# Kernel optimization log

Measured on AMD Instinct MI355X. Metric: run time of the kernel, lower is better.

Reference implementation:

```python
import jax, jax.numpy as jnp
import numpy as np
import math

D_MODEL = 1024
NUM_HEADS = 16


def setup_inputs() -> dict:
    key = jax.random.key(0)
    ks = jax.random.split(key, 5)
    B, S, D = 4, 2048, D_MODEL
    scale = 1.0 / math.sqrt(D)
    x = jax.random.normal(ks[0], (B, S, D), dtype=jnp.float32)
    wq = jax.random.normal(ks[1], (D, D), dtype=jnp.float32) * scale
    wk = jax.random.normal(ks[2], (D, D), dtype=jnp.float32) * scale
    wv = jax.random.normal(ks[3], (D, D), dtype=jnp.float32) * scale
    wo = jax.random.normal(ks[4], (D, D), dtype=jnp.float32) * scale
    return {"x": x, "wq": wq, "wk": wk, "wv": wv, "wo": wo}


def _mhsa(x, wq, wk, wv, wo):
    B, S, D = x.shape
    H = NUM_HEADS
    dk = D // H
    # projections: y = x @ W^T
    q = (x @ wq.T).reshape(B, S, H, dk).transpose(0, 2, 1, 3)  # [B,H,S,dk]
    k = (x @ wk.T).reshape(B, S, H, dk).transpose(0, 2, 1, 3)
    v = (x @ wv.T).reshape(B, S, H, dk).transpose(0, 2, 1, 3)
    scores = jnp.einsum("bhqd,bhkd->bhqk", q, k) / jnp.sqrt(jnp.asarray(dk, x.dtype))
    mask = jnp.tril(jnp.ones((S, S), dtype=bool))  # [S,S] causal
    neg_inf = jnp.asarray(-jnp.inf, scores.dtype)
    scores_masked = jnp.where(mask, scores, neg_inf)
    max_scores = jnp.max(scores_masked, axis=-1, keepdims=True)
    max_scores = jnp.where(jnp.isfinite(max_scores), max_scores, jnp.zeros_like(max_scores))
    exp_scores = jnp.exp(scores - max_scores) * mask.astype(scores.dtype)
    denom = jnp.maximum(exp_scores.sum(axis=-1, keepdims=True), 1e-9)
    attn = exp_scores / denom
    out = jnp.einsum("bhqk,bhkd->bhqd", attn, v)  # [B,H,S,dk]
    out = out.transpose(0, 2, 1, 3).reshape(B, S, D)
    return out @ wo.T


def reference(x, wq, wk, wv, wo):
    return _mhsa(x, wq, wk, wv, wo)
```

## Files before the change

kernel.cpp:

```cpp
#include <hip/hip_runtime.h>
#include <stdint.h>


typedef __attribute__((ext_vector_type(8))) short short8;
typedef __attribute__((ext_vector_type(4))) short short4v;
typedef __attribute__((ext_vector_type(4))) float float4v;
typedef __attribute__((ext_vector_type(2))) unsigned int uint2v;

#define QSCALE 0.18033688011112042f
#define EXP_C2 5.770780163555852f

__device__ inline short f2bf(float f) {
  union { float f; uint32_t u; } v; v.f = f;
  uint32_t r = (v.u + 0x7fffu + ((v.u >> 16) & 1)) >> 16;
  return (short)(uint16_t)r;
}

__device__ inline unsigned int pack2bf(float a, float b) {
  union { float f; unsigned int u; } ua, ub;
  ua.f = a; ub.f = b;
  return __builtin_amdgcn_perm(ub.u, ua.u, 0x07060302u);
}

__device__ inline void async_copy16(const void* g, void* l) {
  __builtin_amdgcn_global_load_lds(
      (const __attribute__((address_space(1))) void*)g,
      (__attribute__((address_space(3))) void*)l, 16, 0, 0);
}

__global__ __launch_bounds__(256) void cvtAll(
    const float* __restrict__ x, const float* __restrict__ wq,
    const float* __restrict__ wk, const float* __restrict__ wv,
    const float* __restrict__ wo,
    short* __restrict__ xb, short* __restrict__ wqb, short* __restrict__ wkb,
    short* __restrict__ wvb, short* __restrict__ wob) {
  const int b = blockIdx.x;
  const float* s; short* d; int base;
  if (b < 8192) { s = x; d = xb; base = b; }
  else {
    const int wi = (b - 8192) >> 10; base = (b - 8192) & 1023;
    s = (wi == 0) ? wq : (wi == 1) ? wk : (wi == 2) ? wv : wo;
    d = (wi == 0) ? wqb : (wi == 1) ? wkb : (wi == 2) ? wvb : wob;
  }
  const size_t i = (size_t)base * 256 + threadIdx.x;
  const float4v v = *(const float4v*)(s + 4 * i);
  short4v o;
  o[0] = f2bf(v[0]); o[1] = f2bf(v[1]);
  o[2] = f2bf(v[2]); o[3] = f2bf(v[3]);
  *(short4v*)(d + 4 * i) = o;
}

template <int MODE>
__global__ __launch_bounds__(256) void gemm_bt(
    const short* __restrict__ A,
    const short* __restrict__ W0, const short* __restrict__ W1,
    const short* __restrict__ W2,
    short* __restrict__ Yb0, short* __restrict__ Yb1, short* __restrict__ Yb2,
    float* __restrict__ Yf) {
  constexpr int Kd = 1024;
  __shared__ __align__(16) short As[2][128 * 32];
  __shared__ __align__(16) short Bs[2][128 * 32];

  const int t = threadIdx.x;
  const int w = t >> 6, l = t & 63, l15 = l & 15, quad = l >> 4;
  const int wm = w >> 1, wn = w & 1;

  int mblk, nblk, zz = 0;
  {
    const int o = blockIdx.x;
    const int xcd = o & 7, slot = o >> 3;
    mblk = (xcd << 3) | (slot & 7);
    const int c = slot >> 3;
    if (MODE == 0) { nblk = c & 7; zz = c >> 3; }
    else nblk = c;
  }
  const int m0 = mblk * 128, n0 = nblk * 128;

  const short* W = W0;
  short* Yb = Yb0;
  float sc = 1.0f;
  if (MODE == 0) {
    if (zz == 0) sc = QSCALE;
    else if (zz == 1) { W = W1; Yb = Yb1; }
    else { W = W2; Yb = Yb2; }
  }

  float4v acc[4][4];
#pragma unroll
  for (int i = 0; i < 4; i++)
#pragma unroll
    for (int j = 0; j < 4; j++) acc[i][j] = (float4v){0.f, 0.f, 0.f, 0.f};

  const int r4 = t >> 2, c48 = (t & 3) * 8;
  const short* Wbase = W + (n0 + r4) * Kd + c48;
  const int ldsW = w * 512;
  const int i0 = m0 + r4;
  const int i1 = m0 + 64 + r4;

  auto STAGE = [&](int k0, int b) {
    if (MODE == 0) {
      async_copy16(A + (size_t)i0 * Kd + k0 + c48, &As[b][ldsW]);
      async_copy16(A + (size_t)i1 * Kd + k0 + c48, &As[b][ldsW + 2048]);
    } else {
      const int k = k0 + c48, h = k >> 6, dd = k & 63;
      async_copy16(A + ((((size_t)(i0 >> 11) * 16 + h) * 2048 + (i0 & 2047)) * 64 + dd),
                   &As[b][ldsW]);
      async_copy16(A + ((((size_t)(i1 >> 11) * 16 + h) * 2048 + (i1 & 2047)) * 64 + dd),
                   &As[b][ldsW + 2048]);
    }
    async_copy16(Wbase + k0, &Bs[b][ldsW]);
    async_copy16(Wbase + 64 * Kd + k0, &Bs[b][ldsW + 2048]);
  };

  STAGE(0, 0);
  __syncthreads();

  for (int k0 = 0; k0 < Kd; k0 += 32) {
    const int cur = (k0 >> 5) & 1;
    if (k0 + 32 < Kd) STAGE(k0 + 32, cur ^ 1);
    short8 af[4], bf[4];
#pragma unroll
    for (int mi = 0; mi < 4; mi++)
      af[mi] = *(const short8*)&As[cur][(wm * 64 + mi * 16 + l15) * 32 + quad * 8];
#pragma unroll
    for (int ni = 0; ni < 4; ni++)
      bf[ni] = *(const short8*)&Bs[cur][(wn * 64 + ni * 16 + l15) * 32 + quad * 8];
#pragma unroll
    for (int mi = 0; mi < 4; mi++)
#pragma unroll
      for (int ni = 0; ni < 4; ni++)
        acc[mi][ni] = __builtin_amdgcn_mfma_f32_16x16x32_bf16(
            af[mi], bf[ni], acc[mi][ni], 0, 0, 0);
    __syncthreads();
  }

#pragma unroll
  for (int mi = 0; mi < 4; mi++) {
    const int ib = m0 + wm * 64 + mi * 16 + quad * 4;
#pragma unroll
    for (int ni = 0; ni < 4; ni++) {
      const int j = n0 + wn * 64 + ni * 16 + l15;
#pragma unroll
      for (int r = 0; r < 4; r++) {
        const int i = ib + r;
        if (MODE == 0) {
          Yb[((((size_t)(i >> 11) * 16 + (j >> 6)) * 2048 + (i & 2047)) * 64 + (j & 63))] =
              f2bf(acc[mi][ni][r] * sc);
        } else {
          Yf[(size_t)i * 1024 + j] = acc[mi][ni][r];
        }
      }
    }
  }
}

__global__ __launch_bounds__(256) void transV(const short* __restrict__ V,
                                              short* __restrict__ VT) {
  __shared__ __align__(16) short Ls[64 * 72];
  const int t = threadIdx.x;
  const int s0 = blockIdx.x * 64, bh = blockIdx.y;
  const short* Vh = V + (size_t)bh * 2048 * 64;
  short* Th = VT + (size_t)bh * 64 * 2048;
  const int r = t >> 2, c = (t & 3) * 16;
  *(short8*)&Ls[r * 72 + c] = *(const short8*)&Vh[(size_t)(s0 + r) * 64 + c];
  *(short8*)&Ls[r * 72 + c + 8] = *(const short8*)&Vh[(size_t)(s0 + r) * 64 + c + 8];
  __syncthreads();
  short8 o0, o1;
#pragma unroll
  for (int j = 0; j < 8; j++) {
    o0[j] = Ls[(c + j) * 72 + r];
    o1[j] = Ls[(c + 8 + j) * 72 + r];
  }
  *(short8*)&Th[(size_t)r * 2048 + s0 + c] = o0;
  *(short8*)&Th[(size_t)r * 2048 + s0 + c + 8] = o1;
}

__global__ __launch_bounds__(256) void attn4(
    short* __restrict__ Q,
    const short* __restrict__ K,
    const short* __restrict__ VT) {
  __shared__ __align__(16) short Ks[2][64 * 64];
  __shared__ __align__(16) short Vs[2][64 * 64];
  __shared__ __align__(16) short Ps[4][16 * 64];

  const int t = threadIdx.x;
  const int w = t >> 6, l = t & 63, l15 = l & 15, quad = l >> 4;
  const int bh = blockIdx.x;
  const int qp = blockIdx.y;
  short* Qh = Q + (size_t)bh * 2048 * 64;
  const short* Kh = K + (size_t)bh * 2048 * 64;
  const short* Vh = VT + (size_t)bh * 64 * 2048;

  const int sr = t >> 2, c0 = t & 3;
  const int ssw = sr & 7;
  const int stA = sr * 64 + (((2 * c0) ^ ssw) << 3);
  const int stB = sr * 64 + (((2 * c0 + 1) ^ ssw) << 3);
  const int gA = c0 * 16, gB = c0 * 16 + 8;

  const int fsw = l15 & 7;
  const int fc0 = (quad ^ fsw) << 3;
  const int fc1 = ((4 + quad) ^ fsw) << 3;
  short* PsW = &Ps[w][0];
  const int pwr = l15 * 64;

  short8 ones;
#pragma unroll
  for (int j = 0; j < 8; j++) ones[j] = (short)0x3F80;
  const float4v initC = (float4v){-EXP_C2, -EXP_C2, -EXP_C2, -EXP_C2};

  for (int pass = 0; pass < 2; pass++) {
    const int q0 = (pass ? (31 - qp) : qp) * 64;
    const int qn = q0 + w * 16 + l15;
    const short8 qf0 = *(const short8*)&Qh[(size_t)qn * 64 + quad * 8];
    const short8 qf1 = *(const short8*)&Qh[(size_t)qn * 64 + 32 + quad * 8];

    float4v acc[4];
#pragma unroll
    for (int dt = 0; dt < 4; dt++) acc[dt] = (float4v){0.f, 0.f, 0.f, 0.f};
    float4v accL = (float4v){0.f, 0.f, 0.f, 0.f};

    short8 kv0 = *(const short8*)&Kh[(size_t)sr * 64 + gA];
    short8 kv1 = *(const short8*)&Kh[(size_t)sr * 64 + gB];
    short8 vv0 = *(const short8*)&Vh[(size_t)sr * 2048 + gA];
    short8 vv1 = *(const short8*)&Vh[(size_t)sr * 2048 + gB];

    int p = 0;
    for (int kb = 0; kb <= q0; kb += 64, p ^= 1) {
      const bool diag = (kb == q0);
      short* KsP = &Ks[p][0];
      short* VsP = &Vs[p][0];
      *(short8*)&KsP[stA] = kv0;
      *(short8*)&KsP[stB] = kv1;
      *(short8*)&VsP[stA] = vv0;
      *(short8*)&VsP[stB] = vv1;
      __syncthreads();

      const int kb2 = diag ? kb : kb + 64;
      kv0 = *(const short8*)&Kh[(size_t)(kb2 + sr) * 64 + gA];
      kv1 = *(const short8*)&Kh[(size_t)(kb2 + sr) * 64 + gB];
      vv0 = *(const short8*)&Vh[(size_t)sr * 2048 + kb2 + gA];
      vv1 = *(const short8*)&Vh[(size_t)sr * 2048 + kb2 + gB];

#pragma unroll
      for (int kt = 0; kt < 4; kt++) {
        const int krb = (kt * 16 + l15) * 64;
        const short8 kf0 = *(const short8*)&KsP[krb + fc0];
        const short8 kf1 = *(const short8*)&KsP[krb + fc1];
        __builtin_amdgcn_s_setprio(1);
        float4v s = __builtin_amdgcn_mfma_f32_16x16x32_bf16(kf0, qf0, initC, 0, 0, 0);
        s = __builtin_amdgcn_mfma_f32_16x16x32_bf16(kf1, qf1, s, 0, 0, 0);
        __builtin_amdgcn_s_setprio(0);
        float p0 = __builtin_amdgcn_exp2f(s[0]);
        float p1 = __builtin_amdgcn_exp2f(s[1]);
        float p2 = __builtin_amdgcn_exp2f(s[2]);
        float p3 = __builtin_amdgcn_exp2f(s[3]);
        if (diag) {
          const int key = kb + kt * 16 + quad * 4;
          p0 = (key <= qn) ? p0 : 0.f;
          p1 = (key + 1 <= qn) ? p1 : 0.f;
          p2 = (key + 2 <= qn) ? p2 : 0.f;
          p3 = (key + 3 <= qn) ? p3 : 0.f;
        }
        uint2v pw;
        pw[0] = pack2bf(p0, p1);
        pw[1] = pack2bf(p2, p3);
        *(uint2v*)&PsW[pwr + (((2 * kt + (quad >> 1)) ^ fsw) << 3) +
                       ((quad & 1) << 2)] = pw;
      }
      __builtin_amdgcn_wave_barrier();

      const short8 pf0 = *(const short8*)&PsW[pwr + fc0];
      const short8 pf1 = *(const short8*)&PsW[pwr + fc1];
      __builtin_amdgcn_s_setprio(1);
#pragma unroll
      for (int dt = 0; dt < 4; dt++) {
        const int vrb = (dt * 16 + l15) * 64;
        const short8 vf0 = *(const short8*)&VsP[vrb + fc0];
        const short8 vf1 = *(const short8*)&VsP[vrb + fc1];
        acc[dt] = __builtin_amdgcn_mfma_f32_16x16x32_bf16(vf0, pf0, acc[dt], 0, 0, 0);
        acc[dt] = __builtin_amdgcn_mfma_f32_16x16x32_bf16(vf1, pf1, acc[dt], 0, 0, 0);
      }
      accL = __builtin_amdgcn_mfma_f32_16x16x32_bf16(ones, pf0, accL, 0, 0, 0);
      accL = __builtin_amdgcn_mfma_f32_16x16x32_bf16(ones, pf1, accL, 0, 0, 0);
      __builtin_amdgcn_s_setprio(0);
    }

    const float inv = 1.0f / fmaxf(accL[0], 1e-30f);
#pragma unroll
    for (int dt = 0; dt < 4; dt++) {
      short4v o;
#pragma unroll
      for (int ri = 0; ri < 4; ri++) o[ri] = f2bf(acc[dt][ri] * inv);
      *(short4v*)&Qh[(size_t)qn * 64 + dt * 16 + quad * 4] = o;
    }
    if (pass == 0) __syncthreads();
  }
}

extern "C" void kernel_launch(void* const* d_in, const int* in_sizes, int n_in,
                              void* d_out, int out_size, void* d_ws,
                              size_t ws_size, hipStream_t stream) {
  const float* x = (const float*)d_in[0];
  const float* wq = (const float*)d_in[1];
  const float* wk = (const float*)d_in[2];
  const float* wv = (const float*)d_in[3];
  const float* wo = (const float*)d_in[4];
  float* out = (float*)d_out;

  short* xb = (short*)d_out;
  short* vtg = xb + (size_t)8192 * 1024;

  short* wqb = (short*)d_ws;
  short* wkb = wqb + (size_t)1024 * 1024;
  short* wvb = wkb + (size_t)1024 * 1024;
  short* wob = wvb + (size_t)1024 * 1024;
  short* qws = wob + (size_t)1024 * 1024;
  short* kws = qws + (size_t)8192 * 1024;
  short* vws = kws + (size_t)8192 * 1024;

  cvtAll<<<12288, 256, 0, stream>>>(x, wq, wk, wv, wo, xb, wqb, wkb, wvb, wob);
  gemm_bt<0><<<1536, 256, 0, stream>>>(
      xb, wqb, wkb, wvb, qws, kws, vws, nullptr);
  transV<<<dim3(32, 64), 256, 0, stream>>>(vws, vtg);
  attn4<<<dim3(64, 16), 256, 0, stream>>>(qws, kws, vtg);
  gemm_bt<1><<<512, 256, 0, stream>>>(
      qws, wob, nullptr, nullptr, nullptr, nullptr, nullptr, out);
}
```

Before: 243.0 us.

## Fuse fp32-to-bf16 conversion of x into the QKV projection GEMM

The separate conversion pass over x (8192x1024 fp32) is removed. The QKV GEMM now loads fp32 x directly into registers, converts it with packed bf16 instructions, and writes it to LDS as part of the double-buffered pipeline. This saves one full read and write of x plus the bf16 re-read, but x is now read three times in fp32 (once per Q/K/V z-slice) and A-tile staging goes through registers instead of async LDS copies.

```diff
diff --git a/kernel.cpp b/kernel.cpp
--- a/kernel.cpp
+++ b/kernel.cpp
@@ -6,6 +6,7 @@
 typedef __attribute__((ext_vector_type(4))) short short4v;
 typedef __attribute__((ext_vector_type(4))) float float4v;
 typedef __attribute__((ext_vector_type(2))) unsigned int uint2v;
+typedef __attribute__((ext_vector_type(4))) unsigned int uint4v;
 
 #define QSCALE 0.18033688011112042f
 #define EXP_C2 5.770780163555852f
@@ -22,26 +23,27 @@
   return __builtin_amdgcn_perm(ub.u, ua.u, 0x07060302u);
 }
 
+__device__ inline unsigned int cvtpk(float a, float b) {
+  unsigned int r;
+  asm("v_cvt_pk_bf16_f32 %0, %1, %2" : "=v"(r) : "v"(a), "v"(b));
+  return r;
+}
+
 __device__ inline void async_copy16(const void* g, void* l) {
   __builtin_amdgcn_global_load_lds(
       (const __attribute__((address_space(1))) void*)g,
       (__attribute__((address_space(3))) void*)l, 16, 0, 0);
 }
 
-__global__ __launch_bounds__(256) void cvtAll(
-    const float* __restrict__ x, const float* __restrict__ wq,
-    const float* __restrict__ wk, const float* __restrict__ wv,
-    const float* __restrict__ wo,
-    short* __restrict__ xb, short* __restrict__ wqb, short* __restrict__ wkb,
+__global__ __launch_bounds__(256) void cvtW(
+    const float* __restrict__ wq, const float* __restrict__ wk,
+    const float* __restrict__ wv, const float* __restrict__ wo,
+    short* __restrict__ wqb, short* __restrict__ wkb,
     short* __restrict__ wvb, short* __restrict__ wob) {
   const int b = blockIdx.x;
-  const float* s; short* d; int base;
-  if (b < 8192) { s = x; d = xb; base = b; }
-  else {
-    const int wi = (b - 8192) >> 10; base = (b - 8192) & 1023;
-    s = (wi == 0) ? wq : (wi == 1) ? wk : (wi == 2) ? wv : wo;
-    d = (wi == 0) ? wqb : (wi == 1) ? wkb : (wi == 2) ? wvb : wob;
-  }
+  const int wi = b >> 10, base = b & 1023;
+  const float* s = (wi == 0) ? wq : (wi == 1) ? wk : (wi == 2) ? wv : wo;
+  short* d = (wi == 0) ? wqb : (wi == 1) ? wkb : (wi == 2) ? wvb : wob;
   const size_t i = (size_t)base * 256 + threadIdx.x;
   const float4v v = *(const float4v*)(s + 4 * i);
   short4v o;
@@ -52,6 +54,7 @@
 
 template <int MODE>
 __global__ __launch_bounds__(256) void gemm_bt(
+    const float* __restrict__ Xf,
     const short* __restrict__ A,
     const short* __restrict__ W0, const short* __restrict__ W1,
     const short* __restrict__ W2,
@@ -96,12 +99,13 @@
   const int ldsW = w * 512;
   const int i0 = m0 + r4;
   const int i1 = m0 + 64 + r4;
-
-  auto STAGE = [&](int k0, int b) {
-    if (MODE == 0) {
-      async_copy16(A + (size_t)i0 * Kd + k0 + c48, &As[b][ldsW]);
-      async_copy16(A + (size_t)i1 * Kd + k0 + c48, &As[b][ldsW + 2048]);
-    } else {
+  const float* X0 = Xf + (size_t)i0 * Kd + c48;
+  const float* X1 = Xf + (size_t)i1 * Kd + c48;
+
+  float4v a0, a1, a2, a3;
+
+  auto STAGE_ASYNC = [&](int k0, int b) {
+    if (MODE == 1) {
       const int k = k0 + c48, h = k >> 6, dd = k & 63;
       async_copy16(A + ((((size_t)(i0 >> 11) * 16 + h) * 2048 + (i0 & 2047)) * 64 + dd),
                    &As[b][ldsW]);
@@ -111,13 +115,33 @@
     async_copy16(Wbase + k0, &Bs[b][ldsW]);
     async_copy16(Wbase + 64 * Kd + k0, &Bs[b][ldsW + 2048]);
   };
-
-  STAGE(0, 0);
+  auto LOADA = [&](int k0) {
+    a0 = *(const float4v*)(X0 + k0);
+    a1 = *(const float4v*)(X0 + k0 + 4);
+    a2 = *(const float4v*)(X1 + k0);
+    a3 = *(const float4v*)(X1 + k0 + 4);
+  };
+  auto WRITEA = [&](int b) {
+    uint4v u0, u1;
+    u0[0] = cvtpk(a0[0], a0[1]); u0[1] = cvtpk(a0[2], a0[3]);
+    u0[2] = cvtpk(a1[0], a1[1]); u0[3] = cvtpk(a1[2], a1[3]);
+    u1[0] = cvtpk(a2[0], a2[1]); u1[1] = cvtpk(a2[2], a2[3]);
+    u1[2] = cvtpk(a3[0], a3[1]); u1[3] = cvtpk(a3[2], a3[3]);
+    *(uint4v*)&As[b][8 * t] = u0;
+    *(uint4v*)&As[b][2048 + 8 * t] = u1;
+  };
+
+  STAGE_ASYNC(0, 0);
+  if (MODE == 0) { LOADA(0); WRITEA(0); }
   __syncthreads();
 
   for (int k0 = 0; k0 < Kd; k0 += 32) {
-    const int cur = (k0 >> 5) & 1;
-    if (k0 + 32 < Kd) STAGE(k0 + 32, cur ^ 1);
+    const int cur = (k0 >> 5) & 1, nxt = cur ^ 1;
+    const bool pre = (k0 + 32 < Kd);
+    if (pre) {
+      STAGE_ASYNC(k0 + 32, nxt);
+      if (MODE == 0) LOADA(k0 + 32);
+    }
     short8 af[4], bf[4];
 #pragma unroll
     for (int mi = 0; mi < 4; mi++)
@@ -131,6 +155,7 @@
       for (int ni = 0; ni < 4; ni++)
         acc[mi][ni] = __builtin_amdgcn_mfma_f32_16x16x32_bf16(
             af[mi], bf[ni], acc[mi][ni], 0, 0, 0);
+    if (MODE == 0 && pre) WRITEA(nxt);
     __syncthreads();
   }
 
@@ -307,8 +332,7 @@
   const float* wo = (const float*)d_in[4];
   float* out = (float*)d_out;
 
-  short* xb = (short*)d_out;
-  short* vtg = xb + (size_t)8192 * 1024;
+  short* vtg = (short*)d_out;
 
   short* wqb = (short*)d_ws;
   short* wkb = wqb + (size_t)1024 * 1024;
@@ -318,11 +342,11 @@
   short* kws = qws + (size_t)8192 * 1024;
   short* vws = kws + (size_t)8192 * 1024;
 
-  cvtAll<<<12288, 256, 0, stream>>>(x, wq, wk, wv, wo, xb, wqb, wkb, wvb, wob);
+  cvtW<<<4096, 256, 0, stream>>>(wq, wk, wv, wo, wqb, wkb, wvb, wob);
   gemm_bt<0><<<1536, 256, 0, stream>>>(
-      xb, wqb, wkb, wvb, qws, kws, vws, nullptr);
+      x, nullptr, wqb, wkb, wvb, qws, kws, vws, nullptr);
   transV<<<dim3(32, 64), 256, 0, stream>>>(vws, vtg);
   attn4<<<dim3(64, 16), 256, 0, stream>>>(qws, kws, vtg);
   gemm_bt<1><<<512, 256, 0, stream>>>(
-      qws, wob, nullptr, nullptr, nullptr, nullptr, nullptr, out);
-}
+      nullptr, qws, wob, nullptr, nullptr, nullptr, nullptr, nullptr, out);
+}
```

Measured after the change: 254.5 us. 4.8% more time.

## Triple-buffer GEMM LDS tiles with swizzled layout and single barrier per step

Applied to the files above, without the earlier changes.

Switches the projection GEMM's shared-memory staging from double to triple buffering. Each k-step now waits with a partial vmcnt instead of a full __syncthreads, so one tile load can stay in flight while the current tile is consumed. The LDS tile is repacked into a 64-wide XOR-swizzled layout to cut bank conflicts on the fragment reads. This uses more LDS, which could lower occupancy, and depends on the vmcnt count being right for correctness.

```diff
diff --git a/kernel.cpp b/kernel.cpp
--- a/kernel.cpp
+++ b/kernel.cpp
@@ -58,8 +58,8 @@
     short* __restrict__ Yb0, short* __restrict__ Yb1, short* __restrict__ Yb2,
     float* __restrict__ Yf) {
   constexpr int Kd = 1024;
-  __shared__ __align__(16) short As[2][128 * 32];
-  __shared__ __align__(16) short Bs[2][128 * 32];
+  __shared__ __align__(16) short As[3][64 * 64];
+  __shared__ __align__(16) short Bs[3][64 * 64];
 
   const int t = threadIdx.x;
   const int w = t >> 6, l = t & 63, l15 = l & 15, quad = l >> 4;
@@ -91,47 +91,65 @@
 #pragma unroll
     for (int j = 0; j < 4; j++) acc[i][j] = (float4v){0.f, 0.f, 0.f, 0.f};
 
-  const int r4 = t >> 2, c48 = (t & 3) * 8;
-  const short* Wbase = W + (n0 + r4) * Kd + c48;
+  const int rr = t >> 3;
+  const int u = (t & 7) ^ (rr & 7);
+  const int mo = rr + ((u >> 2) << 6);
+  const int ko = (u & 3) * 8;
   const int ldsW = w * 512;
-  const int i0 = m0 + r4;
-  const int i1 = m0 + 64 + r4;
+
+  const short* Wp1 = W + (size_t)(n0 + mo) * Kd + ko;
+  const short* Wp2 = W + (size_t)(n0 + 32 + mo) * Kd + ko;
+  const short* Ap1 = A + (size_t)(m0 + mo) * Kd + ko;
+  const short* Ap2 = A + (size_t)(m0 + 32 + mo) * Kd + ko;
+  const int iA1 = m0 + mo, iA2 = m0 + 32 + mo;
 
   auto STAGE = [&](int k0, int b) {
     if (MODE == 0) {
-      async_copy16(A + (size_t)i0 * Kd + k0 + c48, &As[b][ldsW]);
-      async_copy16(A + (size_t)i1 * Kd + k0 + c48, &As[b][ldsW + 2048]);
+      async_copy16(Ap1 + k0, &As[b][ldsW]);
+      async_copy16(Ap2 + k0, &As[b][2048 + ldsW]);
     } else {
-      const int k = k0 + c48, h = k >> 6, dd = k & 63;
-      async_copy16(A + ((((size_t)(i0 >> 11) * 16 + h) * 2048 + (i0 & 2047)) * 64 + dd),
+      const int k = k0 + ko, h = k >> 6, dd = k & 63;
+      async_copy16(A + ((((size_t)(iA1 >> 11) * 16 + h) * 2048 + (iA1 & 2047)) * 64 + dd),
                    &As[b][ldsW]);
-      async_copy16(A + ((((size_t)(i1 >> 11) * 16 + h) * 2048 + (i1 & 2047)) * 64 + dd),
-                   &As[b][ldsW + 2048]);
-    }
-    async_copy16(Wbase + k0, &Bs[b][ldsW]);
-    async_copy16(Wbase + 64 * Kd + k0, &Bs[b][ldsW + 2048]);
+      async_copy16(A + ((((size_t)(iA2 >> 11) * 16 + h) * 2048 + (iA2 & 2047)) * 64 + dd),
+                   &As[b][2048 + ldsW]);
+    }
+    async_copy16(Wp1 + k0, &Bs[b][ldsW]);
+    async_copy16(Wp2 + k0, &Bs[b][2048 + ldsW]);
   };
 
+  const int swz = l15 & 7;
+  const int aCh = (((wm << 2) | quad) ^ swz) << 3;
+  const int bCh = (((wn << 2) | quad) ^ swz) << 3;
+  const int rB = l15 * 64;
+
   STAGE(0, 0);
-  __syncthreads();
-
+
+  int cur = 0;
   for (int k0 = 0; k0 < Kd; k0 += 32) {
-    const int cur = (k0 >> 5) & 1;
-    if (k0 + 32 < Kd) STAGE(k0 + 32, cur ^ 1);
+    const int nxt = (cur == 2) ? 0 : cur + 1;
+    if (k0 + 32 < Kd) {
+      STAGE(k0 + 32, nxt);
+      asm volatile("s_waitcnt vmcnt(4)" ::: "memory");
+    } else {
+      asm volatile("s_waitcnt vmcnt(0)" ::: "memory");
+    }
+    __builtin_amdgcn_s_barrier();
+
     short8 af[4], bf[4];
 #pragma unroll
     for (int mi = 0; mi < 4; mi++)
-      af[mi] = *(const short8*)&As[cur][(wm * 64 + mi * 16 + l15) * 32 + quad * 8];
+      af[mi] = *(const short8*)&As[cur][mi * 1024 + rB + aCh];
 #pragma unroll
     for (int ni = 0; ni < 4; ni++)
-      bf[ni] = *(const short8*)&Bs[cur][(wn * 64 + ni * 16 + l15) * 32 + quad * 8];
+      bf[ni] = *(const short8*)&Bs[cur][ni * 1024 + rB + bCh];
 #pragma unroll
     for (int mi = 0; mi < 4; mi++)
 #pragma unroll
       for (int ni = 0; ni < 4; ni++)
         acc[mi][ni] = __builtin_amdgcn_mfma_f32_16x16x32_bf16(
             af[mi], bf[ni], acc[mi][ni], 0, 0, 0);
-    __syncthreads();
+    cur = nxt;
   }
 
 #pragma unroll
```

New measurement: 249.3 us. 2.6% more time.

## Add 8-wave 256x128 QKV projection GEMM with swizzled LDS and split-phase pipelining

Applied to the files above, without the earlier changes.

Replaces the QKV projection GEMM with a dedicated kernel using 512 threads, 256x128 tiles, and a 64-wide K step split into two 32-wide sub-phases. It adds an XOR-swizzled LDS layout, explicit vmcnt waits with raw barriers so loads overlap MFMA work, and s_setprio around the MFMA blocks. The goal is better operand reuse, fewer LDS bank conflicts and fewer full syncs in the largest GEMM. The cost is more LDS per block and hand-tuned waitcnt logic that must match the number of copies in flight.

```diff
diff --git a/kernel.cpp b/kernel.cpp
--- a/kernel.cpp
+++ b/kernel.cpp
@@ -50,12 +50,126 @@
   *(short4v*)(d + 4 * i) = o;
 }
 
+__global__ __launch_bounds__(512) void gemm_qkv8(
+    const short* __restrict__ A,
+    const short* __restrict__ W0, const short* __restrict__ W1,
+    const short* __restrict__ W2,
+    short* __restrict__ Yb0, short* __restrict__ Yb1, short* __restrict__ Yb2) {
+  constexpr int Kd = 1024;
+  __shared__ __align__(16) short As[2 * 2 * 2 * 4096];
+  __shared__ __align__(16) short Bs[2 * 2 * 4096];
+
+  const int t = threadIdx.x;
+  const int wv = t >> 6, l = t & 63, l15 = l & 15, quad = l >> 4;
+  const int wm = wv >> 1, wn = wv & 1;
+
+  int mblk, nblk, zz;
+  {
+    const int o = blockIdx.x;
+    const int xcd = o & 7, slot = o >> 3;
+    mblk = (xcd << 2) | (slot & 3);
+    const int c = slot >> 2;
+    nblk = c & 7; zz = c >> 3;
+  }
+  const int m0 = mblk * 256, n0 = nblk * 128;
+
+  const short* W = W0;
+  short* Yb = Yb0;
+  float sc = 1.0f;
+  if (zz == 0) sc = QSCALE;
+  else if (zz == 1) { W = W1; Yb = Yb1; }
+  else { W = W2; Yb = Yb2; }
+
+  float4v acc[4][4];
+#pragma unroll
+  for (int i = 0; i < 4; i++)
+#pragma unroll
+    for (int j = 0; j < 4; j++) acc[i][j] = (float4v){0.f, 0.f, 0.f, 0.f};
+
+  const int rr = t >> 3, j8 = t & 7;
+  const int u = j8 ^ (rr & 7);
+  const int mo = rr + ((u >> 2) << 6);
+  const int ko = (u & 3) * 8;
+  const int dstW = wv * 512;
+
+  const short* Asrc0 = A + (size_t)(m0 + mo) * Kd + ko;
+  const short* Asrc1 = A + (size_t)(m0 + 128 + mo) * Kd + ko;
+  const short* Bsrc = W + (size_t)(n0 + mo) * Kd + ko;
+
+  auto STAGE_S = [&](int kbase, int b, int s) {
+    async_copy16(Asrc0 + kbase, &As[((b * 2 + s) * 2 + 0) * 4096 + dstW]);
+    async_copy16(Asrc1 + kbase, &As[((b * 2 + s) * 2 + 1) * 4096 + dstW]);
+    async_copy16(Bsrc + kbase, &Bs[(b * 2 + s) * 4096 + dstW]);
+  };
+
+  const int swz = l15 & 7;
+  const int aBase = (wm >> 1) * 4096 + l15 * 64 +
+                    (((((wm & 1) << 2) | quad) ^ swz) << 3);
+  const int bBase = l15 * 64 + ((((wn << 2) | quad) ^ swz) << 3);
+
+  auto PHASE = [&](int cur, int sl) {
+    const int ab = cur * 16384 + sl * 8192 + aBase;
+    const int bb = cur * 8192 + sl * 4096 + bBase;
+    short8 af[4], bf[4];
+#pragma unroll
+    for (int mi = 0; mi < 4; mi++) af[mi] = *(const short8*)&As[ab + mi * 1024];
+#pragma unroll
+    for (int ni = 0; ni < 4; ni++) bf[ni] = *(const short8*)&Bs[bb + ni * 1024];
+    __builtin_amdgcn_s_setprio(1);
+#pragma unroll
+    for (int mi = 0; mi < 4; mi++)
+#pragma unroll
+      for (int ni = 0; ni < 4; ni++)
+        acc[mi][ni] = __builtin_amdgcn_mfma_f32_16x16x32_bf16(
+            af[mi], bf[ni], acc[mi][ni], 0, 0, 0);
+    __builtin_amdgcn_s_setprio(0);
+  };
+
+  STAGE_S(0, 0, 0);
+  STAGE_S(32, 0, 1);
+
+  for (int kt = 0; kt < 16; ++kt) {
+    const int cur = kt & 1, nb = cur ^ 1;
+    const int k0 = kt * 64;
+    const bool last = (kt == 15);
+
+    if (!last) {
+      STAGE_S(k0 + 64, nb, 0);
+      asm volatile("s_waitcnt vmcnt(3)" ::: "memory");
+    } else {
+      asm volatile("s_waitcnt vmcnt(0)" ::: "memory");
+    }
+    __builtin_amdgcn_s_barrier();
+    __builtin_amdgcn_sched_barrier(0);
+    PHASE(cur, 0);
+
+    if (!last) STAGE_S(k0 + 96, nb, 1);
+    PHASE(cur, 1);
+
+    __builtin_amdgcn_s_barrier();
+    __builtin_amdgcn_sched_barrier(0);
+  }
+
+#pragma unroll
+  for (int mi = 0; mi < 4; mi++) {
+    const int ib = m0 + wm * 64 + mi * 16 + quad * 4;
+#pragma unroll
+    for (int ni = 0; ni < 4; ni++) {
+      const int j = n0 + wn * 64 + ni * 16 + l15;
+#pragma unroll
+      for (int r = 0; r < 4; r++) {
+        const int i = ib + r;
+        Yb[((((size_t)(i >> 11) * 16 + (j >> 6)) * 2048 + (i & 2047)) * 64 + (j & 63))] =
+            f2bf(acc[mi][ni][r] * sc);
+      }
+    }
+  }
+}
+
 template <int MODE>
 __global__ __launch_bounds__(256) void gemm_bt(
     const short* __restrict__ A,
-    const short* __restrict__ W0, const short* __restrict__ W1,
-    const short* __restrict__ W2,
-    short* __restrict__ Yb0, short* __restrict__ Yb1, short* __restrict__ Yb2,
+    const short* __restrict__ W0,
     float* __restrict__ Yf) {
   constexpr int Kd = 1024;
   __shared__ __align__(16) short As[2][128 * 32];
@@ -65,25 +179,16 @@
   const int w = t >> 6, l = t & 63, l15 = l & 15, quad = l >> 4;
   const int wm = w >> 1, wn = w & 1;
 
-  int mblk, nblk, zz = 0;
+  int mblk, nblk;
   {
     const int o = blockIdx.x;
     const int xcd = o & 7, slot = o >> 3;
     mblk = (xcd << 3) | (slot & 7);
-    const int c = slot >> 3;
-    if (MODE == 0) { nblk = c & 7; zz = c >> 3; }
-    else nblk = c;
+    nblk = slot >> 3;
   }
   const int m0 = mblk * 128, n0 = nblk * 128;
 
   const short* W = W0;
-  short* Yb = Yb0;
-  float sc = 1.0f;
-  if (MODE == 0) {
-    if (zz == 0) sc = QSCALE;
-    else if (zz == 1) { W = W1; Yb = Yb1; }
-    else { W = W2; Yb = Yb2; }
-  }
 
   float4v acc[4][4];
 #pragma unroll
@@ -98,16 +203,11 @@
   const int i1 = m0 + 64 + r4;
 
   auto STAGE = [&](int k0, int b) {
-    if (MODE == 0) {
-      async_copy16(A + (size_t)i0 * Kd + k0 + c48, &As[b][ldsW]);
-      async_copy16(A + (size_t)i1 * Kd + k0 + c48, &As[b][ldsW + 2048]);
-    } else {
-      const int k = k0 + c48, h = k >> 6, dd = k & 63;
-      async_copy16(A + ((((size_t)(i0 >> 11) * 16 + h) * 2048 + (i0 & 2047)) * 64 + dd),
-                   &As[b][ldsW]);
-      async_copy16(A + ((((size_t)(i1 >> 11) * 16 + h) * 2048 + (i1 & 2047)) * 64 + dd),
-                   &As[b][ldsW + 2048]);
-    }
+    const int k = k0 + c48, h = k >> 6, dd = k & 63;
+    async_copy16(A + ((((size_t)(i0 >> 11) * 16 + h) * 2048 + (i0 & 2047)) * 64 + dd),
+                 &As[b][ldsW]);
+    async_copy16(A + ((((size_t)(i1 >> 11) * 16 + h) * 2048 + (i1 & 2047)) * 64 + dd),
+                 &As[b][ldsW + 2048]);
     async_copy16(Wbase + k0, &Bs[b][ldsW]);
     async_copy16(Wbase + 64 * Kd + k0, &Bs[b][ldsW + 2048]);
   };
@@ -143,12 +243,7 @@
 #pragma unroll
       for (int r = 0; r < 4; r++) {
         const int i = ib + r;
-        if (MODE == 0) {
-          Yb[((((size_t)(i >> 11) * 16 + (j >> 6)) * 2048 + (i & 2047)) * 64 + (j & 63))] =
-              f2bf(acc[mi][ni][r] * sc);
-        } else {
-          Yf[(size_t)i * 1024 + j] = acc[mi][ni][r];
-        }
+        Yf[(size_t)i * 1024 + j] = acc[mi][ni][r];
       }
     }
   }
@@ -319,10 +414,10 @@
   short* vws = kws + (size_t)8192 * 1024;
 
   cvtAll<<<12288, 256, 0, stream>>>(x, wq, wk, wv, wo, xb, wqb, wkb, wvb, wob);
-  gemm_bt<0><<<1536, 256, 0, stream>>>(
-      xb, wqb, wkb, wvb, qws, kws, vws, nullptr);
+  gemm_qkv8<<<768, 512, 0, stream>>>(
+      xb, wqb, wkb, wvb, qws, kws, vws);
   transV<<<dim3(32, 64), 256, 0, stream>>>(vws, vtg);
   attn4<<<dim3(64, 16), 256, 0, stream>>>(qws, kws, vtg);
   gemm_bt<1><<<512, 256, 0, stream>>>(
-      qws, wob, nullptr, nullptr, nullptr, nullptr, nullptr, out);
-}
+      qws, wob, out);
+}
```

New measurement: 257.2 us. 5.9% more time.
